# Kernel optimization log

Measured on AMD Instinct MI355X. Metric: run time of the kernel, lower is better.

The kernel has to match this reference:

```python
import jax, jax.numpy as jnp
import numpy as np

N, E, C, O, H, W, K = 32, 512, 64, 128, 64, 64, 3


def setup_inputs() -> dict:
    key = jax.random.key(0)
    k1, k2, k3, k4, k5, k6 = jax.random.split(key, 6)
    scale_w = 1.0 / np.sqrt(E)
    return {
        "embedding": jax.random.normal(k1, (N, E), dtype=jnp.float32),
        "images": jax.random.normal(k2, (N, C, H, W), dtype=jnp.float32),
        "w_weight": jax.random.uniform(k3, (O * C * K * K, E), dtype=jnp.float32, minval=-scale_w, maxval=scale_w),
        "w_bias": jax.random.uniform(k4, (O * C * K * K,), dtype=jnp.float32, minval=-scale_w, maxval=scale_w),
        "b_weight": jax.random.uniform(k5, (O, E), dtype=jnp.float32, minval=-scale_w, maxval=scale_w),
        "b_bias": jax.random.uniform(k6, (O,), dtype=jnp.float32, minval=-scale_w, maxval=scale_w),
    }


def reference(embedding, images, w_weight, w_bias, b_weight, b_bias):
    n, c, h, w = images.shape
    o = b_bias.shape[0]
    # per-sample generated filters and biases
    c1_w = embedding @ w_weight.T + w_bias          # [N, O*C*K*K]
    c1_b = embedding @ b_weight.T + b_bias          # [N, O]
    filt = c1_w.reshape(n, o, c, K, K)              # matches torch view(O, C*K*K)
    # im2col equivalent: pad then gather 3x3 shifted views -> [N,C,K,K,H,W]
    xp = jnp.pad(images, ((0, 0), (0, 0), (1, 1), (1, 1)))
    patches = jnp.stack(
        [xp[:, :, i:i + h, j:j + w] for i in range(K) for j in range(K)], axis=2
    ).reshape(n, c, K, K, h, w)
    out = jnp.einsum('nocij,ncijhw->nohw', filt, patches)
    return out + c1_b[:, :, None, None]
```

## Files before the change

### kernel.cpp

```cpp
#include <hip/hip_runtime.h>
#include <hip/hip_bf16.h>

#define N_  32
#define E_  512
#define C_  64
#define O_  128
#define H_  64
#define W_  64
#define CK9 576
#define M_  (O_*CK9)

typedef __bf16 bf16x8 __attribute__((ext_vector_type(8)));
typedef float  f32x4  __attribute__((ext_vector_type(4)));

__device__ inline bf16x8 cvt8(const float* p) {
    f32x4 lo = *reinterpret_cast<const f32x4*>(p);
    f32x4 hi = *reinterpret_cast<const f32x4*>(p + 4);
    bf16x8 r;
    r[0] = (__bf16)lo[0]; r[1] = (__bf16)lo[1]; r[2] = (__bf16)lo[2]; r[3] = (__bf16)lo[3];
    r[4] = (__bf16)hi[0]; r[5] = (__bf16)hi[1]; r[6] = (__bf16)hi[2]; r[7] = (__bf16)hi[3];
    return r;
}

__global__ __launch_bounds__(256) void gen_filters(
    const float* __restrict__ emb, const float* __restrict__ w_weight,
    const float* __restrict__ w_bias, __bf16* __restrict__ filt)
{
    int tid  = threadIdx.x;
    int wave = tid >> 6, lane = tid & 63;
    int quad = lane >> 4, l16 = lane & 15;
    int m0 = blockIdx.x * 64 + wave * 16;

    f32x4 acc0 = {0.f,0.f,0.f,0.f};
    f32x4 acc1 = {0.f,0.f,0.f,0.f};

    const float* arow = w_weight + (size_t)(m0 + l16) * E_ + quad * 8;
    const float* b0p  = emb + (size_t)l16 * E_ + quad * 8;
    const float* b1p  = emb + (size_t)(l16 + 16) * E_ + quad * 8;

#pragma unroll
    for (int k0 = 0; k0 < E_; k0 += 32) {
        bf16x8 a  = cvt8(arow + k0);
        bf16x8 b0 = cvt8(b0p + k0);
        bf16x8 b1 = cvt8(b1p + k0);
        acc0 = __builtin_amdgcn_mfma_f32_16x16x32_bf16(a, b0, acc0, 0, 0, 0);
        acc1 = __builtin_amdgcn_mfma_f32_16x16x32_bf16(a, b1, acc1, 0, 0, 0);
    }

#pragma unroll
    for (int r = 0; r < 4; r++) {
        int m = m0 + quad * 4 + r;
        int o = m / 576;
        int rem = m - o * 576;
        int c = rem / 9;
        int t = rem - c * 9;
        size_t base = (size_t)o * 576 + t * 64 + c;
        float bias = w_bias[m];
        filt[(size_t)l16        * M_ + base] = (__bf16)(acc0[r] + bias);
        filt[(size_t)(l16 + 16) * M_ + base] = (__bf16)(acc1[r] + bias);
    }
}

__global__ __launch_bounds__(256) void gen_bias(
    const float* __restrict__ emb, const float* __restrict__ b_weight,
    const float* __restrict__ b_bias, float* __restrict__ c1b)
{
    int wid  = (blockIdx.x * 256 + threadIdx.x) >> 6;
    int lane = threadIdx.x & 63;
    int n = wid >> 7, o = wid & 127;
    const float* e = emb + (size_t)n * E_ + lane * 8;
    const float* b = b_weight + (size_t)o * E_ + lane * 8;
    f32x4 e0 = *reinterpret_cast<const f32x4*>(e);
    f32x4 e1 = *reinterpret_cast<const f32x4*>(e + 4);
    f32x4 w0 = *reinterpret_cast<const f32x4*>(b);
    f32x4 w1 = *reinterpret_cast<const f32x4*>(b + 4);
    float s = e0[0]*w0[0] + e0[1]*w0[1] + e0[2]*w0[2] + e0[3]*w0[3]
            + e1[0]*w1[0] + e1[1]*w1[1] + e1[2]*w1[2] + e1[3]*w1[3];
#pragma unroll
    for (int off = 32; off; off >>= 1) s += __shfl_xor(s, off, 64);
    if (lane == 0) c1b[wid] = s + b_bias[o];
}

__device__ __forceinline__ void load_a(bf16x8* dst, const __bf16* fA, int k0) {
#pragma unroll
    for (int mi = 0; mi < 4; mi++)
        dst[mi] = *reinterpret_cast<const bf16x8*>(fA + (size_t)mi * 16 * CK9 + k0);
}

__device__ __forceinline__ void load_b(bf16x8* dst, const __bf16* slab,
                                       int wn, int l16, int quad, int k0) {
    int t  = k0 >> 6;
    int di = t / 3;
    int tj = t - di * 3;
    int c0 = k0 & 32;
#pragma unroll
    for (int ni = 0; ni < 4; ni++) {
        int col = ni * 16 + l16 + tj;
        dst[ni] = *reinterpret_cast<const bf16x8*>(
            slab + ((wn + di) * 66 + col) * 72 + c0 + quad * 8);
    }
}

__global__ __launch_bounds__(256) void conv_gemm(
    const float* __restrict__ img, const __bf16* __restrict__ filt,
    const float* __restrict__ c1b, float* __restrict__ out)
{
    __shared__ __align__(16) __bf16 slab[4 * 66 * 72];

    int tid  = threadIdx.x;
    int wave = tid >> 6, lane = tid & 63;
    int quad = lane >> 4, l16 = lane & 15;
    int wm = wave & 1, wn = wave >> 1;

    int blk = blockIdx.x;
    int xcd = blk & 7, jj = blk >> 3;
    int n  = (xcd << 2) + (jj & 3);
    int pt = jj >> 2;
    int p0 = pt << 7;
    int h0 = pt << 1;

    const float* imgn = img + (size_t)n * (C_ * H_ * W_);
    for (int idx = tid; idx < 4 * 66 * 64; idx += 256) {
        int col = idx % 66;
        int rc  = idx / 66;
        int c   = rc & 63;
        int r   = rc >> 6;
        int hh  = h0 - 1 + r;
        int w   = col - 1;
        float v = 0.f;
        if ((unsigned)hh < 64u && (unsigned)w < 64u)
            v = imgn[((size_t)c << 12) + (hh << 6) + w];
        slab[(r * 66 + col) * 72 + c] = (__bf16)v;
    }

    f32x4 acc[4][4];
#pragma unroll
    for (int mi = 0; mi < 4; mi++)
#pragma unroll
        for (int ni = 0; ni < 4; ni++)
            acc[mi][ni] = (f32x4){0.f, 0.f, 0.f, 0.f};

    const __bf16* fA = filt + (size_t)n * M_ + (size_t)(wm * 64 + l16) * CK9 + quad * 8;

    __syncthreads();

    bf16x8 aA[4], bA[4], aB[4], bB[4];
    load_a(aA, fA, 0);
    load_b(bA, slab, wn, l16, quad, 0);

#define MFMA16(av, bv)                                                        \
    {                                                                         \
        _Pragma("unroll")                                                     \
        for (int mi = 0; mi < 4; mi++)                                        \
            _Pragma("unroll")                                                 \
            for (int ni = 0; ni < 4; ni++)                                    \
                acc[mi][ni] = __builtin_amdgcn_mfma_f32_16x16x32_bf16(        \
                    (av)[mi], (bv)[ni], acc[mi][ni], 0, 0, 0);                \
    }

#pragma unroll
    for (int k = 0; k < 18; k += 2) {
        if (k + 1 < 18) {
            load_a(aB, fA, (k + 1) * 32);
            load_b(bB, slab, wn, l16, quad, (k + 1) * 32);
        }
        MFMA16(aA, bA);
        if (k + 2 < 18) {
            load_a(aA, fA, (k + 2) * 32);
            load_b(bA, slab, wn, l16, quad, (k + 2) * 32);
        }
        MFMA16(aB, bB);
    }
#undef MFMA16

#pragma unroll
    for (int mi = 0; mi < 4; mi++) {
#pragma unroll
        for (int r = 0; r < 4; r++) {
            int o = wm * 64 + mi * 16 + quad * 4 + r;
            float bias = c1b[(n << 7) + o];
            float* op = out + (((size_t)(n << 7) + o) << 12) + p0 + wn * 64 + l16;
#pragma unroll
            for (int ni = 0; ni < 4; ni++)
                op[ni * 16] = acc[mi][ni][r] + bias;
        }
    }
}

extern "C" void kernel_launch(void* const* d_in, const int* in_sizes, int n_in,
                              void* d_out, int out_size, void* d_ws, size_t ws_size,
                              hipStream_t stream)
{
    (void)in_sizes; (void)n_in; (void)out_size; (void)ws_size;
    const float* emb      = (const float*)d_in[0];
    const float* images   = (const float*)d_in[1];
    const float* w_weight = (const float*)d_in[2];
    const float* w_bias   = (const float*)d_in[3];
    const float* b_weight = (const float*)d_in[4];
    const float* b_bias   = (const float*)d_in[5];
    float* out = (float*)d_out;

    __bf16* filt = (__bf16*)d_ws;
    float*  c1b  = (float*)((char*)d_ws + (size_t)N_ * M_ * 2);

    gen_filters<<<dim3(M_ / 64), dim3(256), 0, stream>>>(emb, w_weight, w_bias, filt);
    gen_bias<<<dim3(N_ * O_ / 4), dim3(256), 0, stream>>>(emb, b_weight, b_bias, c1b);
    conv_gemm<<<dim3(N_ * 32), dim3(256), 0, stream>>>(images, filt, c1b, out);
}
```

Before: 371.2 us.

## Stage gen_filters operands in LDS and restructure conv_gemm tiling per wave

gen_filters now converts the embedding once into LDS and stages 128-row weight tiles in shared memory, so each block computes a 128x32 output tile and embedding reads are no longer repeated through global memory. conv_gemm changes its wave layout so each wave covers 32 output channels and all 128 pixels, and it preloads the filter registers per half of K. Each block now processes two pixel strips, with vectorized float4 image loads and explicit zeroing of the padding columns. The trade-offs are more accumulator and A-operand registers (which can lower occupancy), half as many conv blocks, and extra barriers in the filter GEMM loop.

```diff
diff --git a/kernel.cpp b/kernel.cpp
--- a/kernel.cpp
+++ b/kernel.cpp
@@ -11,53 +11,81 @@
 #define M_  (O_*CK9)
 
 typedef __bf16 bf16x8 __attribute__((ext_vector_type(8)));
+typedef __bf16 bf16x4 __attribute__((ext_vector_type(4)));
 typedef float  f32x4  __attribute__((ext_vector_type(4)));
-
-__device__ inline bf16x8 cvt8(const float* p) {
-    f32x4 lo = *reinterpret_cast<const f32x4*>(p);
-    f32x4 hi = *reinterpret_cast<const f32x4*>(p + 4);
-    bf16x8 r;
-    r[0] = (__bf16)lo[0]; r[1] = (__bf16)lo[1]; r[2] = (__bf16)lo[2]; r[3] = (__bf16)lo[3];
-    r[4] = (__bf16)hi[0]; r[5] = (__bf16)hi[1]; r[6] = (__bf16)hi[2]; r[7] = (__bf16)hi[3];
-    return r;
-}
 
 __global__ __launch_bounds__(256) void gen_filters(
     const float* __restrict__ emb, const float* __restrict__ w_weight,
     const float* __restrict__ w_bias, __bf16* __restrict__ filt)
 {
+    __shared__ __align__(16) __bf16 embS[32 * 520];
+    __shared__ __align__(16) __bf16 wS[128 * 40];
+
     int tid  = threadIdx.x;
     int wave = tid >> 6, lane = tid & 63;
     int quad = lane >> 4, l16 = lane & 15;
-    int m0 = blockIdx.x * 64 + wave * 16;
-
-    f32x4 acc0 = {0.f,0.f,0.f,0.f};
-    f32x4 acc1 = {0.f,0.f,0.f,0.f};
-
-    const float* arow = w_weight + (size_t)(m0 + l16) * E_ + quad * 8;
-    const float* b0p  = emb + (size_t)l16 * E_ + quad * 8;
-    const float* b1p  = emb + (size_t)(l16 + 16) * E_ + quad * 8;
-
-#pragma unroll
-    for (int k0 = 0; k0 < E_; k0 += 32) {
-        bf16x8 a  = cvt8(arow + k0);
-        bf16x8 b0 = cvt8(b0p + k0);
-        bf16x8 b1 = cvt8(b1p + k0);
-        acc0 = __builtin_amdgcn_mfma_f32_16x16x32_bf16(a, b0, acc0, 0, 0, 0);
-        acc1 = __builtin_amdgcn_mfma_f32_16x16x32_bf16(a, b1, acc1, 0, 0, 0);
-    }
-
-#pragma unroll
-    for (int r = 0; r < 4; r++) {
-        int m = m0 + quad * 4 + r;
-        int o = m / 576;
-        int rem = m - o * 576;
-        int c = rem / 9;
-        int t = rem - c * 9;
-        size_t base = (size_t)o * 576 + t * 64 + c;
-        float bias = w_bias[m];
-        filt[(size_t)l16        * M_ + base] = (__bf16)(acc0[r] + bias);
-        filt[(size_t)(l16 + 16) * M_ + base] = (__bf16)(acc1[r] + bias);
+    int m0 = blockIdx.x * 128;
+
+#pragma unroll
+    for (int i = 0; i < 16; i++) {
+        int idx = (i * 256 + tid) * 4;
+        int n = idx >> 9, e = idx & 511;
+        f32x4 v = *reinterpret_cast<const f32x4*>(emb + n * 512 + e);
+        bf16x4 b;
+        b[0] = (__bf16)v[0]; b[1] = (__bf16)v[1]; b[2] = (__bf16)v[2]; b[3] = (__bf16)v[3];
+        *reinterpret_cast<bf16x4*>(&embS[n * 520 + e]) = b;
+    }
+
+    f32x4 acc[2][2];
+#pragma unroll
+    for (int mi = 0; mi < 2; mi++)
+#pragma unroll
+        for (int ni = 0; ni < 2; ni++)
+            acc[mi][ni] = (f32x4){0.f, 0.f, 0.f, 0.f};
+
+    int sub = tid & 7, rbase = tid >> 3;
+
+    for (int kk = 0; kk < 16; kk++) {
+        int k0 = kk * 32;
+        __syncthreads();
+#pragma unroll
+        for (int q = 0; q < 4; q++) {
+            int row = rbase + q * 32;
+            f32x4 v = *reinterpret_cast<const f32x4*>(
+                w_weight + (size_t)(m0 + row) * 512 + k0 + sub * 4);
+            bf16x4 b;
+            b[0] = (__bf16)v[0]; b[1] = (__bf16)v[1]; b[2] = (__bf16)v[2]; b[3] = (__bf16)v[3];
+            *reinterpret_cast<bf16x4*>(&wS[row * 40 + sub * 4]) = b;
+        }
+        __syncthreads();
+
+        bf16x8 a0 = *reinterpret_cast<const bf16x8*>(&wS[(wave * 32 + l16) * 40 + quad * 8]);
+        bf16x8 a1 = *reinterpret_cast<const bf16x8*>(&wS[(wave * 32 + 16 + l16) * 40 + quad * 8]);
+        bf16x8 b0 = *reinterpret_cast<const bf16x8*>(&embS[l16 * 520 + k0 + quad * 8]);
+        bf16x8 b1 = *reinterpret_cast<const bf16x8*>(&embS[(16 + l16) * 520 + k0 + quad * 8]);
+        acc[0][0] = __builtin_amdgcn_mfma_f32_16x16x32_bf16(a0, b0, acc[0][0], 0, 0, 0);
+        acc[0][1] = __builtin_amdgcn_mfma_f32_16x16x32_bf16(a0, b1, acc[0][1], 0, 0, 0);
+        acc[1][0] = __builtin_amdgcn_mfma_f32_16x16x32_bf16(a1, b0, acc[1][0], 0, 0, 0);
+        acc[1][1] = __builtin_amdgcn_mfma_f32_16x16x32_bf16(a1, b1, acc[1][1], 0, 0, 0);
+    }
+
+#pragma unroll
+    for (int mi = 0; mi < 2; mi++) {
+#pragma unroll
+        for (int r = 0; r < 4; r++) {
+            int m = m0 + wave * 32 + mi * 16 + quad * 4 + r;
+            int o = m / 576;
+            int rem = m - o * 576;
+            int c = rem / 9;
+            int t = rem - c * 9;
+            size_t base = (size_t)o * 576 + t * 64 + c;
+            float bias = w_bias[m];
+#pragma unroll
+            for (int ni = 0; ni < 2; ni++) {
+                int n = ni * 16 + l16;
+                filt[(size_t)n * M_ + base] = (__bf16)(acc[mi][ni][r] + bias);
+            }
+        }
     }
 }
 
@@ -81,26 +109,6 @@
     if (lane == 0) c1b[wid] = s + b_bias[o];
 }
 
-__device__ __forceinline__ void load_a(bf16x8* dst, const __bf16* fA, int k0) {
-#pragma unroll
-    for (int mi = 0; mi < 4; mi++)
-        dst[mi] = *reinterpret_cast<const bf16x8*>(fA + (size_t)mi * 16 * CK9 + k0);
-}
-
-__device__ __forceinline__ void load_b(bf16x8* dst, const __bf16* slab,
-                                       int wn, int l16, int quad, int k0) {
-    int t  = k0 >> 6;
-    int di = t / 3;
-    int tj = t - di * 3;
-    int c0 = k0 & 32;
-#pragma unroll
-    for (int ni = 0; ni < 4; ni++) {
-        int col = ni * 16 + l16 + tj;
-        dst[ni] = *reinterpret_cast<const bf16x8*>(
-            slab + ((wn + di) * 66 + col) * 72 + c0 + quad * 8);
-    }
-}
-
 __global__ __launch_bounds__(256) void conv_gemm(
     const float* __restrict__ img, const __bf16* __restrict__ filt,
     const float* __restrict__ c1b, float* __restrict__ out)
@@ -110,79 +118,98 @@
     int tid  = threadIdx.x;
     int wave = tid >> 6, lane = tid & 63;
     int quad = lane >> 4, l16 = lane & 15;
-    int wm = wave & 1, wn = wave >> 1;
 
     int blk = blockIdx.x;
-    int xcd = blk & 7, jj = blk >> 3;
-    int n  = (xcd << 2) + (jj & 3);
-    int pt = jj >> 2;
-    int p0 = pt << 7;
-    int h0 = pt << 1;
+    int n     = ((blk & 7) << 2) + ((blk >> 3) & 3);
+    int strip = blk >> 5;
 
     const float* imgn = img + (size_t)n * (C_ * H_ * W_);
-    for (int idx = tid; idx < 4 * 66 * 64; idx += 256) {
-        int col = idx % 66;
-        int rc  = idx / 66;
-        int c   = rc & 63;
-        int r   = rc >> 6;
-        int hh  = h0 - 1 + r;
-        int w   = col - 1;
-        float v = 0.f;
-        if ((unsigned)hh < 64u && (unsigned)w < 64u)
-            v = imgn[((size_t)c << 12) + (hh << 6) + w];
-        slab[(r * 66 + col) * 72 + c] = (__bf16)v;
-    }
-
-    f32x4 acc[4][4];
-#pragma unroll
-    for (int mi = 0; mi < 4; mi++)
-#pragma unroll
-        for (int ni = 0; ni < 4; ni++)
-            acc[mi][ni] = (f32x4){0.f, 0.f, 0.f, 0.f};
-
-    const __bf16* fA = filt + (size_t)n * M_ + (size_t)(wm * 64 + l16) * CK9 + quad * 8;
-
-    __syncthreads();
-
-    bf16x8 aA[4], bA[4], aB[4], bB[4];
-    load_a(aA, fA, 0);
-    load_b(bA, slab, wn, l16, quad, 0);
-
-#define MFMA16(av, bv)                                                        \
-    {                                                                         \
-        _Pragma("unroll")                                                     \
-        for (int mi = 0; mi < 4; mi++)                                        \
-            _Pragma("unroll")                                                 \
-            for (int ni = 0; ni < 4; ni++)                                    \
-                acc[mi][ni] = __builtin_amdgcn_mfma_f32_16x16x32_bf16(        \
-                    (av)[mi], (bv)[ni], acc[mi][ni], 0, 0, 0);                \
-    }
-
-#pragma unroll
-    for (int k = 0; k < 18; k += 2) {
-        if (k + 1 < 18) {
-            load_a(aB, fA, (k + 1) * 32);
-            load_b(bB, slab, wn, l16, quad, (k + 1) * 32);
-        }
-        MFMA16(aA, bA);
-        if (k + 2 < 18) {
-            load_a(aA, fA, (k + 2) * 32);
-            load_b(bA, slab, wn, l16, quad, (k + 2) * 32);
-        }
-        MFMA16(aB, bB);
-    }
-#undef MFMA16
-
-#pragma unroll
-    for (int mi = 0; mi < 4; mi++) {
-#pragma unroll
-        for (int r = 0; r < 4; r++) {
-            int o = wm * 64 + mi * 16 + quad * 4 + r;
-            float bias = c1b[(n << 7) + o];
-            float* op = out + (((size_t)(n << 7) + o) << 12) + p0 + wn * 64 + l16;
-#pragma unroll
-            for (int ni = 0; ni < 4; ni++)
-                op[ni * 16] = acc[mi][ni][r] + bias;
+    const __bf16* fBase = filt + (size_t)n * M_ + (size_t)(wave * 32 + l16) * CK9 + quad * 8;
+
+    for (int pt2 = 0; pt2 < 2; pt2++) {
+        int pt = strip * 2 + pt2;
+        int h0 = pt * 2;
+
+        __syncthreads();
+
+#pragma unroll
+        for (int i = 0; i < 16; i++) {
+            int idx = i * 256 + tid;
+            int wq  = (idx & 15) * 4;
+            int rc  = idx >> 4;
+            int r = rc >> 6, c = rc & 63;
+            int hh = h0 - 1 + r;
+            f32x4 v = {0.f, 0.f, 0.f, 0.f};
+            if ((unsigned)hh < 64u)
+                v = *reinterpret_cast<const f32x4*>(imgn + ((size_t)c << 12) + (hh << 6) + wq);
+            __bf16* d = &slab[(r * 66 + wq + 1) * 72 + c];
+            d[0]   = (__bf16)v[0];
+            d[72]  = (__bf16)v[1];
+            d[144] = (__bf16)v[2];
+            d[216] = (__bf16)v[3];
+        }
+#pragma unroll
+        for (int idx = tid; idx < 512; idx += 256) {
+            int cc = idx & 63, rj = idx >> 6;
+            int r = rj >> 1, col = (rj & 1) * 65;
+            slab[(r * 66 + col) * 72 + cc] = (__bf16)0.f;
+        }
+        __syncthreads();
+
+        f32x4 acc[2][8];
+#pragma unroll
+        for (int mi = 0; mi < 2; mi++)
+#pragma unroll
+            for (int ni = 0; ni < 8; ni++)
+                acc[mi][ni] = (f32x4){0.f, 0.f, 0.f, 0.f};
+
+#pragma unroll
+        for (int kh = 0; kh < 2; kh++) {
+            bf16x8 aR[2][9];
+#pragma unroll
+            for (int mi = 0; mi < 2; mi++)
+#pragma unroll
+                for (int t9 = 0; t9 < 9; t9++)
+                    aR[mi][t9] = *reinterpret_cast<const bf16x8*>(
+                        fBase + (size_t)mi * 16 * CK9 + kh * 288 + t9 * 32);
+
+#pragma unroll
+            for (int t9 = 0; t9 < 9; t9++) {
+                int kk = kh * 9 + t9;
+                int k0 = kk * 32;
+                int t  = k0 >> 6;
+                int di = t / 3;
+                int tj = t - 3 * di;
+                int c0 = k0 & 32;
+
+                bf16x8 b[8];
+#pragma unroll
+                for (int ni = 0; ni < 8; ni++) {
+                    int lh = ni >> 2;
+                    int w  = (ni & 3) * 16 + l16;
+                    b[ni] = *reinterpret_cast<const bf16x8*>(
+                        &slab[((lh + di) * 66 + w + tj) * 72 + c0 + quad * 8]);
+                }
+#pragma unroll
+                for (int mi = 0; mi < 2; mi++)
+#pragma unroll
+                    for (int ni = 0; ni < 8; ni++)
+                        acc[mi][ni] = __builtin_amdgcn_mfma_f32_16x16x32_bf16(
+                            aR[mi][t9], b[ni], acc[mi][ni], 0, 0, 0);
+            }
+        }
+
+#pragma unroll
+        for (int mi = 0; mi < 2; mi++) {
+#pragma unroll
+            for (int r = 0; r < 4; r++) {
+                int o = wave * 32 + mi * 16 + quad * 4 + r;
+                float bias = c1b[(n << 7) + o];
+                float* op = out + (((size_t)(n << 7) + o) << 12) + (pt << 7);
+#pragma unroll
+                for (int ni = 0; ni < 8; ni++)
+                    op[(ni >> 2) * 64 + (ni & 3) * 16 + l16] = acc[mi][ni][r] + bias;
+            }
         }
     }
 }
@@ -203,7 +230,7 @@
     __bf16* filt = (__bf16*)d_ws;
     float*  c1b  = (float*)((char*)d_ws + (size_t)N_ * M_ * 2);
 
-    gen_filters<<<dim3(M_ / 64), dim3(256), 0, stream>>>(emb, w_weight, w_bias, filt);
+    gen_filters<<<dim3(M_ / 128), dim3(256), 0, stream>>>(emb, w_weight, w_bias, filt);
     gen_bias<<<dim3(N_ * O_ / 4), dim3(256), 0, stream>>>(emb, b_weight, b_bias, c1b);
-    conv_gemm<<<dim3(N_ * 32), dim3(256), 0, stream>>>(images, filt, c1b, out);
-}
+    conv_gemm<<<dim3(512), dim3(256), 0, stream>>>(images, filt, c1b, out);
+}
```

Result: faster. 331.2 us (-10.8%).
